# Performance work log

Hardware: AMD Instinct MI355X
Metric: run time of the kernel (lower is better)

Reference implementation:

```python
import jax, jax.numpy as jnp
import numpy as np


def _edt(mask_zero):
    """Exact 2D Euclidean distance transform: distance of every pixel to the
    nearest True pixel in mask_zero (matches scipy.ndimage.distance_transform_edt
    applied to the one-hot map, where background pixels are zeros).
    mask_zero: [B, C, H, W] bool, True where the one-hot map is 0.
    Returns float32 [B, C, H, W].
    """
    B, C, H, W = mask_zero.shape
    BIG = jnp.float32(H + W)  # larger than any in-image 1D distance

    # Phase 1: 1D distance to nearest zero along axis H (forward + backward scans)
    def step(d, m):  # d,m: [B, C, W]
        d = jnp.where(m, 0.0, d + 1.0)
        return d, d

    m_rows = jnp.moveaxis(mask_zero, 2, 0)  # [H, B, C, W]
    init = jnp.full((B, C, W), BIG, dtype=jnp.float32)
    _, g_f = jax.lax.scan(step, init, m_rows)
    _, g_b = jax.lax.scan(step, init, m_rows[::-1])
    g = jnp.minimum(g_f, g_b[::-1])          # [H, B, C, W]
    g = jnp.moveaxis(g, 0, 2)                # [B, C, H, W]

    # Phase 2: exact combine along axis W: d2[.., i, j] = min_k g[.., i, k]^2 + (j-k)^2
    j = jnp.arange(W, dtype=jnp.float32)
    sq = (j[:, None] - j[None, :]) ** 2      # [W(j), W(k)]
    d2 = jnp.min(g[..., None, :] ** 2 + sq, axis=-1)  # [B, C, H, W]
    return jnp.sqrt(d2)


def _rrwmap(y_, num_classes):
    labels = y_[:, 0]  # [B, H, W]
    # one-hot channel c is zero where label != c
    mask_zero = labels[:, None, :, :] != jnp.arange(num_classes)[None, :, None, None]
    d = _edt(mask_zero)                                  # [B, C, H, W]
    maxd = jnp.max(d, axis=(2, 3), keepdims=True)        # per (b, c) max
    rrw = -(d / (maxd + 1e-15))
    return jnp.where(rrw == 0.0, 1.0, rrw)


def setup_inputs() -> dict:
    key = jax.random.key(0)
    k1, k2 = jax.random.split(key)
    B, C, H, W = 2, 4, 256, 256
    x = jax.random.normal(k1, (B, C, H, W), dtype=jnp.float32)
    y_ = jax.random.randint(k2, (B, 1, H, W), 0, C, dtype=jnp.int64)
    return {"x": x, "y_": y_}


def reference(x, y_):
    C = x.shape[1]
    rrw = _rrwmap(y_, C)
    p = jax.nn.softmax(x, axis=1)
    return jnp.mean(p * rrw)
```

## Files before the change

### kernel.cpp

```cpp
#include <hip/hip_runtime.h>

#define B_ 2
#define C_ 4
#define H_ 256
#define W_ 256
constexpr int BC    = B_ * C_;
constexpr int HW    = H_ * W_;
constexpr int NROWS = B_ * H_;
constexpr int NTOT  = B_ * C_ * HW;
constexpr float BIGF = (float)(H_ + W_);

__global__ __launch_bounds__(256) void rows_kernel(
    const int* __restrict__ lab, const float* __restrict__ x,
    float* __restrict__ ps4, float* __restrict__ pm4, float* __restrict__ pa) {
    const int r = blockIdx.x;
    const int b = r >> 8;
    const int i = r & (H_ - 1);
    const int j = threadIdx.x;

    const int* lrow = lab + b * HW + i * W_;
    const int  c    = lrow[j];

    const float* xp = x + b * C_ * HW + i * W_ + j;
    const float x0 = xp[0 * HW], x1 = xp[1 * HW], x2 = xp[2 * HW], x3 = xp[3 * HW];

    const int* lcol = lab + b * HW + j;
    float gu = -1.0f, gd = -1.0f;
    for (int k = 1; gu < 0.0f || gd < 0.0f; ++k) {
        if (gu < 0.0f) {
            const int rr = i - k;
            if (rr < 0) gu = BIGF + (float)(i + 1);
            else if (lcol[rr * W_] != c) gu = (float)k;
        }
        if (gd < 0.0f) {
            const int rr = i + k;
            if (rr >= H_) gd = BIGF + (float)(H_ - i);
            else if (lcol[rr * W_] != c) gd = (float)k;
        }
    }
    const float g = fminf(gu, gd);

    __shared__ int   ls[W_];
    __shared__ float g2s[W_];
    ls[j]  = c;
    g2s[j] = g * g;
    __syncthreads();

    float best = g * g;
    for (int dj = 1; dj < W_; ++dj) {
        const float dd = (float)(dj * dj);
        if (dd >= best) break;
        const int l = j - dj, rr = j + dj;
        if (l >= 0) {
            const float v = (ls[l] == c ? g2s[l] : 0.0f) + dd;
            best = fminf(best, v);
        }
        if (rr < W_) {
            const float v = (ls[rr] == c ? g2s[rr] : 0.0f) + dd;
            best = fminf(best, v);
        }
    }

    const float mx = fmaxf(fmaxf(x0, x1), fmaxf(x2, x3));
    const float e0 = __expf(x0 - mx), e1 = __expf(x1 - mx);
    const float e2 = __expf(x2 - mx), e3 = __expf(x3 - mx);
    const float s  = e0 + e1 + e2 + e3;
    const float ec = (c == 0) ? e0 : (c == 1) ? e1 : (c == 2) ? e2 : e3;
    const float pc = ec / s;

    float va = (s - ec) / s;
    const float psv = pc * sqrtf(best);
    float s0 = (c == 0) ? psv : 0.0f, s1 = (c == 1) ? psv : 0.0f;
    float s2 = (c == 2) ? psv : 0.0f, s3 = (c == 3) ? psv : 0.0f;
    float m0 = (c == 0) ? best : 0.0f, m1 = (c == 1) ? best : 0.0f;
    float m2 = (c == 2) ? best : 0.0f, m3 = (c == 3) ? best : 0.0f;

    #pragma unroll
    for (int off = 32; off; off >>= 1) {
        va += __shfl_down(va, off, 64);
        s0 += __shfl_down(s0, off, 64);
        s1 += __shfl_down(s1, off, 64);
        s2 += __shfl_down(s2, off, 64);
        s3 += __shfl_down(s3, off, 64);
        m0 = fmaxf(m0, __shfl_down(m0, off, 64));
        m1 = fmaxf(m1, __shfl_down(m1, off, 64));
        m2 = fmaxf(m2, __shfl_down(m2, off, 64));
        m3 = fmaxf(m3, __shfl_down(m3, off, 64));
    }
    __shared__ float lred[4][9];
    const int lane = j & 63, wid = j >> 6;
    if (lane == 0) {
        lred[wid][0] = va;
        lred[wid][1] = s0; lred[wid][2] = s1; lred[wid][3] = s2; lred[wid][4] = s3;
        lred[wid][5] = m0; lred[wid][6] = m1; lred[wid][7] = m2; lred[wid][8] = m3;
    }
    __syncthreads();
    if (j == 0) {
        float A = 0.0f, S0 = 0.0f, S1 = 0.0f, S2 = 0.0f, S3 = 0.0f;
        float M0 = 0.0f, M1 = 0.0f, M2 = 0.0f, M3 = 0.0f;
        #pragma unroll
        for (int w = 0; w < 4; ++w) {
            A  += lred[w][0];
            S0 += lred[w][1]; S1 += lred[w][2]; S2 += lred[w][3]; S3 += lred[w][4];
            M0 = fmaxf(M0, lred[w][5]); M1 = fmaxf(M1, lred[w][6]);
            M2 = fmaxf(M2, lred[w][7]); M3 = fmaxf(M3, lred[w][8]);
        }
        ((float4*)ps4)[r] = make_float4(S0, S1, S2, S3);
        ((float4*)pm4)[r] = make_float4(M0, M1, M2, M3);
        pa[r] = A;
    }
}

__global__ __launch_bounds__(256) void final_kernel(
    const float4* __restrict__ ps4, const float4* __restrict__ pm4,
    const float* __restrict__ pa, float* __restrict__ out) {
    const int t = threadIdx.x;
    const int lane = t & 63, wid = t >> 6;
    __shared__ float lred[4][9];
    float total = 0.0f;
    for (int b = 0; b < B_; ++b) {
        const int r = b * H_ + t;
        float4 s4 = ps4[r];
        float4 m4 = pm4[r];
        float  a  = pa[r];
        #pragma unroll
        for (int off = 32; off; off >>= 1) {
            a    += __shfl_down(a, off, 64);
            s4.x += __shfl_down(s4.x, off, 64);
            s4.y += __shfl_down(s4.y, off, 64);
            s4.z += __shfl_down(s4.z, off, 64);
            s4.w += __shfl_down(s4.w, off, 64);
            m4.x = fmaxf(m4.x, __shfl_down(m4.x, off, 64));
            m4.y = fmaxf(m4.y, __shfl_down(m4.y, off, 64));
            m4.z = fmaxf(m4.z, __shfl_down(m4.z, off, 64));
            m4.w = fmaxf(m4.w, __shfl_down(m4.w, off, 64));
        }
        __syncthreads();
        if (lane == 0) {
            lred[wid][0] = a;
            lred[wid][1] = s4.x; lred[wid][2] = s4.y;
            lred[wid][3] = s4.z; lred[wid][4] = s4.w;
            lred[wid][5] = m4.x; lred[wid][6] = m4.y;
            lred[wid][7] = m4.z; lred[wid][8] = m4.w;
        }
        __syncthreads();
        if (t == 0) {
            float A = 0.0f, S0 = 0.0f, S1 = 0.0f, S2 = 0.0f, S3 = 0.0f;
            float M0 = 0.0f, M1 = 0.0f, M2 = 0.0f, M3 = 0.0f;
            #pragma unroll
            for (int w = 0; w < 4; ++w) {
                A  += lred[w][0];
                S0 += lred[w][1]; S1 += lred[w][2]; S2 += lred[w][3]; S3 += lred[w][4];
                M0 = fmaxf(M0, lred[w][5]); M1 = fmaxf(M1, lred[w][6]);
                M2 = fmaxf(M2, lred[w][7]); M3 = fmaxf(M3, lred[w][8]);
            }
            total += A - S0 / (sqrtf(M0) + 1e-15f) - S1 / (sqrtf(M1) + 1e-15f)
                       - S2 / (sqrtf(M2) + 1e-15f) - S3 / (sqrtf(M3) + 1e-15f);
        }
    }
    if (t == 0) out[0] = total / (float)NTOT;
}

extern "C" void kernel_launch(void* const* d_in, const int* in_sizes, int n_in,
                              void* d_out, int out_size, void* d_ws, size_t ws_size,
                              hipStream_t stream) {
    const float* x = (const float*)d_in[0];
    const int*   y = (const int*)d_in[1];
    float* out = (float*)d_out;

    float* ps4 = (float*)d_ws;
    float* pm4 = ps4 + NROWS * 4;
    float* pa  = pm4 + NROWS * 4;

    rows_kernel<<<NROWS, W_, 0, stream>>>(y, x, ps4, pm4, pa);
    final_kernel<<<1, 256, 0, stream>>>((const float4*)ps4, (const float4*)pm4, pa, out);
}
```

Before: 63.86 us.

## Fuse final reduction into rows kernel via global atomics and last-block pattern

Removes the separate final reduction kernel. Each block atomically accumulates its per-class sums and maxima into a small control struct, and the last block to finish, found with an atomic counter, computes the output. This saves one kernel launch but adds a memset node plus atomic contention on a few addresses, and the float atomic adds make the result order-dependent.

Result: slower. 117.8 us (+84.5%).

```diff
diff --git a/kernel.cpp b/kernel.cpp
--- a/kernel.cpp
+++ b/kernel.cpp
@@ -10,9 +10,16 @@
 constexpr int NTOT  = B_ * C_ * HW;
 constexpr float BIGF = (float)(H_ + W_);
 
+struct Ctrl {
+    float        gS[BC];
+    unsigned int gM[BC];
+    float        gA;
+    unsigned int counter;
+};
+
 __global__ __launch_bounds__(256) void rows_kernel(
     const int* __restrict__ lab, const float* __restrict__ x,
-    float* __restrict__ ps4, float* __restrict__ pm4, float* __restrict__ pa) {
+    Ctrl* __restrict__ ctrl, float* __restrict__ out) {
     const int r = blockIdx.x;
     const int b = r >> 8;
     const int i = r & (H_ - 1);
@@ -105,60 +112,29 @@
             M0 = fmaxf(M0, lred[w][5]); M1 = fmaxf(M1, lred[w][6]);
             M2 = fmaxf(M2, lred[w][7]); M3 = fmaxf(M3, lred[w][8]);
         }
-        ((float4*)ps4)[r] = make_float4(S0, S1, S2, S3);
-        ((float4*)pm4)[r] = make_float4(M0, M1, M2, M3);
-        pa[r] = A;
-    }
-}
-
-__global__ __launch_bounds__(256) void final_kernel(
-    const float4* __restrict__ ps4, const float4* __restrict__ pm4,
-    const float* __restrict__ pa, float* __restrict__ out) {
-    const int t = threadIdx.x;
-    const int lane = t & 63, wid = t >> 6;
-    __shared__ float lred[4][9];
-    float total = 0.0f;
-    for (int b = 0; b < B_; ++b) {
-        const int r = b * H_ + t;
-        float4 s4 = ps4[r];
-        float4 m4 = pm4[r];
-        float  a  = pa[r];
-        #pragma unroll
-        for (int off = 32; off; off >>= 1) {
-            a    += __shfl_down(a, off, 64);
-            s4.x += __shfl_down(s4.x, off, 64);
-            s4.y += __shfl_down(s4.y, off, 64);
-            s4.z += __shfl_down(s4.z, off, 64);
-            s4.w += __shfl_down(s4.w, off, 64);
-            m4.x = fmaxf(m4.x, __shfl_down(m4.x, off, 64));
-            m4.y = fmaxf(m4.y, __shfl_down(m4.y, off, 64));
-            m4.z = fmaxf(m4.z, __shfl_down(m4.z, off, 64));
-            m4.w = fmaxf(m4.w, __shfl_down(m4.w, off, 64));
-        }
-        __syncthreads();
-        if (lane == 0) {
-            lred[wid][0] = a;
-            lred[wid][1] = s4.x; lred[wid][2] = s4.y;
-            lred[wid][3] = s4.z; lred[wid][4] = s4.w;
-            lred[wid][5] = m4.x; lred[wid][6] = m4.y;
-            lred[wid][7] = m4.z; lred[wid][8] = m4.w;
-        }
-        __syncthreads();
-        if (t == 0) {
-            float A = 0.0f, S0 = 0.0f, S1 = 0.0f, S2 = 0.0f, S3 = 0.0f;
-            float M0 = 0.0f, M1 = 0.0f, M2 = 0.0f, M3 = 0.0f;
+        const int cb = b * C_;
+        atomicAdd(&ctrl->gA, A);
+        atomicAdd(&ctrl->gS[cb + 0], S0);
+        atomicAdd(&ctrl->gS[cb + 1], S1);
+        atomicAdd(&ctrl->gS[cb + 2], S2);
+        atomicAdd(&ctrl->gS[cb + 3], S3);
+        atomicMax(&ctrl->gM[cb + 0], __float_as_uint(M0));
+        atomicMax(&ctrl->gM[cb + 1], __float_as_uint(M1));
+        atomicMax(&ctrl->gM[cb + 2], __float_as_uint(M2));
+        atomicMax(&ctrl->gM[cb + 3], __float_as_uint(M3));
+        __threadfence();
+        const unsigned int done = atomicAdd(&ctrl->counter, 1u);
+        if (done == (unsigned int)(NROWS - 1)) {
+            float total = atomicAdd(&ctrl->gA, 0.0f);
             #pragma unroll
-            for (int w = 0; w < 4; ++w) {
-                A  += lred[w][0];
-                S0 += lred[w][1]; S1 += lred[w][2]; S2 += lred[w][3]; S3 += lred[w][4];
-                M0 = fmaxf(M0, lred[w][5]); M1 = fmaxf(M1, lred[w][6]);
-                M2 = fmaxf(M2, lred[w][7]); M3 = fmaxf(M3, lred[w][8]);
+            for (int k = 0; k < BC; ++k) {
+                const float Sk = atomicAdd(&ctrl->gS[k], 0.0f);
+                const float Mk = __uint_as_float(atomicAdd(&ctrl->gM[k], 0u));
+                total -= Sk / (sqrtf(Mk) + 1e-15f);
             }
-            total += A - S0 / (sqrtf(M0) + 1e-15f) - S1 / (sqrtf(M1) + 1e-15f)
-                       - S2 / (sqrtf(M2) + 1e-15f) - S3 / (sqrtf(M3) + 1e-15f);
+            out[0] = total / (float)NTOT;
         }
     }
-    if (t == 0) out[0] = total / (float)NTOT;
 }
 
 extern "C" void kernel_launch(void* const* d_in, const int* in_sizes, int n_in,
@@ -167,11 +143,8 @@
     const float* x = (const float*)d_in[0];
     const int*   y = (const int*)d_in[1];
     float* out = (float*)d_out;
+    Ctrl* ctrl = (Ctrl*)d_ws;
 
-    float* ps4 = (float*)d_ws;
-    float* pm4 = ps4 + NROWS * 4;
-    float* pa  = pm4 + NROWS * 4;
-
-    rows_kernel<<<NROWS, W_, 0, stream>>>(y, x, ps4, pm4, pa);
-    final_kernel<<<1, 256, 0, stream>>>((const float4*)ps4, (const float4*)pm4, pa, out);
+    hipMemsetAsync(ctrl, 0, sizeof(Ctrl), stream);
+    rows_kernel<<<NROWS, W_, 0, stream>>>(y, x, ctrl, out);
 }
```
